# Kernel tuning notes

Measured on AMD Instinct MI355X. Metric: run time of the kernel, lower is better.

Reference implementation:

```python
import jax, jax.numpy as jnp
import numpy as np
import math

NUM_HEADS = 16
HIDDEN = 1024
MLP = 4096
SEQ = 2048
HEAD_DIM = HIDDEN // NUM_HEADS  # 64
EPS = 1e-5


def setup_inputs() -> dict:
    key = jax.random.key(0)
    ks = jax.random.split(key, 16)
    s = 0.02
    inp = {
        "x": jax.random.normal(ks[0], (SEQ, HIDDEN), jnp.float32),
        "rope_cos": jnp.cos(jnp.arange(SEQ, dtype=jnp.float32)[:, None] * (1.0 / (10000.0 ** (jnp.arange(HEAD_DIM // 2, dtype=jnp.float32) * 2 / HEAD_DIM)))[None, :]),
        "rope_sin": jnp.sin(jnp.arange(SEQ, dtype=jnp.float32)[:, None] * (1.0 / (10000.0 ** (jnp.arange(HEAD_DIM // 2, dtype=jnp.float32) * 2 / HEAD_DIM)))[None, :]),
        "norm0_w": jnp.ones((HIDDEN,), jnp.float32),
        "norm0_b": jnp.zeros((HIDDEN,), jnp.float32),
        "norm1_w": jnp.ones((HIDDEN,), jnp.float32),
        "norm1_b": jnp.zeros((HIDDEN,), jnp.float32),
        "wqkv_w": jax.random.normal(ks[1], (3 * HIDDEN, HIDDEN), jnp.float32) * s,
        "wqkv_b": jnp.zeros((3 * HIDDEN,), jnp.float32),
        "wo_w": jax.random.normal(ks[2], (HIDDEN, HIDDEN), jnp.float32) * s,
        "wo_b": jnp.zeros((HIDDEN,), jnp.float32),
        "up_w": jax.random.normal(ks[3], (MLP, HIDDEN), jnp.float32) * s,
        "up_b": jnp.zeros((MLP,), jnp.float32),
        "down_w": jax.random.normal(ks[4], (HIDDEN, MLP), jnp.float32) * s,
        "down_b": jnp.zeros((HIDDEN,), jnp.float32),
        # 4 packed sequences of length 512 each
        "input_row_offsets": jnp.array([0, 512, 1024, 1536, 2048], jnp.int32),
    }
    return inp


def _layernorm(x, w, b):
    m = jnp.mean(x, axis=-1, keepdims=True)
    v = jnp.mean((x - m) ** 2, axis=-1, keepdims=True)
    return (x - m) * jax.lax.rsqrt(v + EPS) * w + b


def _rope(t, cos, sin):
    # t: [S, nh, hd]; cos/sin: [S, hd/2] -> complex rotation of adjacent pairs
    S, nh, hd = t.shape
    t2 = t.reshape(S, nh, hd // 2, 2)
    re, im = t2[..., 0], t2[..., 1]
    c = cos[:, None, :]
    s = sin[:, None, :]
    out = jnp.stack([re * c - im * s, re * s + im * c], axis=-1)
    return out.reshape(S, nh, hd)


def _block(x, rope_cos, rope_sin, norm0_w, norm0_b, wqkv_w, wqkv_b, wo_w, wo_b,
           up_w, up_b, down_w, down_b, norm1_w, norm1_b, input_row_offsets):
    S, H = x.shape
    nh, hd = NUM_HEADS, HEAD_DIM
    h = _layernorm(x, norm0_w, norm0_b)
    qkv = (h @ wqkv_w.T + wqkv_b).reshape(S, 3, nh, hd)
    q, k, v = qkv[:, 0], qkv[:, 1], qkv[:, 2]
    q = _rope(q, rope_cos, rope_sin)
    k = _rope(k, rope_cos, rope_sin)
    # block-diagonal bool mask added as 0/1 float (matches torch `attn_weight += bool_mask`)
    seg = jnp.searchsorted(input_row_offsets, jnp.arange(S), side="right") - 1
    mask = (seg[:, None] == seg[None, :]).astype(jnp.float32)  # [S, S]
    scores = jnp.einsum("shd,thd->hst", q, k) / math.sqrt(hd) + mask[None]
    attn = jax.nn.softmax(scores.astype(jnp.float32), axis=-1).astype(q.dtype)
    out = jnp.einsum("hst,thd->shd", attn, v).reshape(S, H)
    x = x + (out @ wo_w.T + wo_b)
    h = _layernorm(x, norm1_w, norm1_b)
    h = jax.nn.gelu(h @ up_w.T + up_b, approximate=True)
    return x + (h @ down_w.T + down_b)


def reference(x, rope_cos, rope_sin, norm0_w, norm0_b, norm1_w, norm1_b,
              wqkv_w, wqkv_b, wo_w, wo_b, up_w, up_b, down_w, down_b,
              input_row_offsets):
    return _block(x, rope_cos, rope_sin, norm0_w, norm0_b, wqkv_w, wqkv_b,
                  wo_w, wo_b, up_w, up_b, down_w, down_b, norm1_w, norm1_b,
                  input_row_offsets)
```

## Files before the change

### kernel.cpp

```cpp
#include <hip/hip_runtime.h>
#include <hip/hip_bf16.h>
#include <math.h>

#define SEQ 2048
#define HID 1024
#define NH 16
#define HD 64

using f32x4  = __attribute__((ext_vector_type(4))) float;
using bf16x8 = __attribute__((ext_vector_type(8))) short;

union U8 { unsigned int u[4]; bf16x8 v; short s[8]; };

__device__ __forceinline__ short f2bf(float f) {
  unsigned int x = __float_as_uint(f);
  unsigned int r = (x + 0x7fffu + ((x >> 16) & 1u)) >> 16;
  return (short)(r & 0xffffu);
}

__device__ __forceinline__ unsigned int pkbf(float a, float b) {
  return ((unsigned int)(unsigned short)f2bf(a)) |
         (((unsigned int)(unsigned short)f2bf(b)) << 16);
}

__device__ __forceinline__ float bf2f_lo(unsigned int u) {
  return __uint_as_float((u & 0xffffu) << 16);
}
__device__ __forceinline__ float bf2f_hi(unsigned int u) {
  return __uint_as_float(u & 0xffff0000u);
}

__device__ __forceinline__ float fast_exp2(float x) {
#if __has_builtin(__builtin_amdgcn_exp2f)
  return __builtin_amdgcn_exp2f(x);
#else
  return exp2f(x);
#endif
}

__device__ __forceinline__ float fast_rcp(float x) {
#if __has_builtin(__builtin_amdgcn_rcpf)
  return __builtin_amdgcn_rcpf(x);
#else
  return 1.0f / x;
#endif
}

__device__ __forceinline__ void async_cp16(const void* g, void* l) {
  __builtin_amdgcn_global_load_lds(
      (__attribute__((address_space(1))) void*)(g),
      (__attribute__((address_space(3))) void*)(l), 16, 0, 0);
}

__global__ void cvt_all_kernel(const float* __restrict__ a, const float* __restrict__ b,
                               const float* __restrict__ c, const float* __restrict__ d,
                               short* __restrict__ oa, short* __restrict__ ob,
                               short* __restrict__ oc, short* __restrict__ od) {
  int i = blockIdx.x * blockDim.x + threadIdx.x;
  const float* src; short* dst; int off;
  if (i < 786432)        { src = a; dst = oa; off = i; }
  else if (i < 1048576)  { src = b; dst = ob; off = i - 786432; }
  else if (i < 2097152)  { src = c; dst = oc; off = i - 1048576; }
  else                   { src = d; dst = od; off = i - 2097152; }
  float4 v = ((const float4*)src)[off];
  short4 o;
  o.x = f2bf(v.x); o.y = f2bf(v.y); o.z = f2bf(v.z); o.w = f2bf(v.w);
  ((short4*)dst)[off] = o;
}

__global__ __launch_bounds__(256) void ln_kernel(const float* __restrict__ x,
    const float* __restrict__ w, const float* __restrict__ b, short* __restrict__ out) {
  int row = blockIdx.x;
  int tid = threadIdx.x;
  float4 v = ((const float4*)(x + (size_t)row * HID))[tid];
  float s  = v.x + v.y + v.z + v.w;
  float s2 = v.x*v.x + v.y*v.y + v.z*v.z + v.w*v.w;
#pragma unroll
  for (int o = 32; o >= 1; o >>= 1) {
    s  += __shfl_xor(s,  o);
    s2 += __shfl_xor(s2, o);
  }
  __shared__ float red[8];
  int wv = tid >> 6;
  if ((tid & 63) == 0) { red[wv] = s; red[4 + wv] = s2; }
  __syncthreads();
  float ts  = red[0] + red[1] + red[2] + red[3];
  float ts2 = red[4] + red[5] + red[6] + red[7];
  float mean = ts * (1.0f / HID);
  float var  = ts2 * (1.0f / HID) - mean * mean;
  float rs = rsqrtf(var + 1e-5f);
  float4 wv4 = ((const float4*)w)[tid];
  float4 bv4 = ((const float4*)b)[tid];
  short4 o;
  o.x = f2bf((v.x - mean) * rs * wv4.x + bv4.x);
  o.y = f2bf((v.y - mean) * rs * wv4.y + bv4.y);
  o.z = f2bf((v.z - mean) * rs * wv4.z + bv4.z);
  o.w = f2bf((v.w - mean) * rs * wv4.w + bv4.w);
  ((short4*)(out + (size_t)row * HID))[tid] = o;
}

__global__ __launch_bounds__(256) void ropev_kernel(const short* __restrict__ qkvb,
    const float* __restrict__ cosb, const float* __restrict__ sinb,
    short* __restrict__ Qh, short* __restrict__ Kh, short* __restrict__ Vt) {
  __shared__ short tile[64 * 72];
  int s0   = blockIdx.x * 64;
  int head = blockIdx.y;
  int tid  = threadIdx.x;
#pragma unroll
  for (int p = 0; p < 2; p++) {
    int seg = p * 256 + tid;
    int row = seg >> 3;
    int c8  = seg & 7;
    bf16x8 v = *(const bf16x8*)(qkvb + (size_t)(s0 + row) * 3072 + 2048 + head * 64 + c8 * 8);
    *(bf16x8*)(tile + row * 72 + c8 * 8) = v;
  }
  int sl = tid >> 3;
  int c  = tid & 7;
#pragma unroll
  for (int j = 0; j < 2; j++) {
    float scale = (j == 0) ? 0.18033688011112043f : 1.0f;
    short* dstm = (j == 0) ? Qh : Kh;
#pragma unroll
    for (int half = 0; half < 2; half++) {
      int s = s0 + half * 32 + sl;
      uint4 uu = *(const uint4*)(qkvb + (size_t)s * 3072 + j * 1024 + head * 64 + c * 8);
      float4 cs = *(const float4*)(cosb + s * 32 + c * 4);
      float4 sn = *(const float4*)(sinb + s * 32 + c * 4);
      uint4 oo;
      {
        float a = bf2f_lo(uu.x), b = bf2f_hi(uu.x);
        oo.x = pkbf(scale * (a * cs.x - b * sn.x), scale * (a * sn.x + b * cs.x));
        a = bf2f_lo(uu.y); b = bf2f_hi(uu.y);
        oo.y = pkbf(scale * (a * cs.y - b * sn.y), scale * (a * sn.y + b * cs.y));
        a = bf2f_lo(uu.z); b = bf2f_hi(uu.z);
        oo.z = pkbf(scale * (a * cs.z - b * sn.z), scale * (a * sn.z + b * cs.z));
        a = bf2f_lo(uu.w); b = bf2f_hi(uu.w);
        oo.w = pkbf(scale * (a * cs.w - b * sn.w), scale * (a * sn.w + b * cs.w));
      }
      *(uint4*)(dstm + ((size_t)head * SEQ + s) * HD + c * 8) = oo;
    }
  }
  __syncthreads();
#pragma unroll
  for (int p = 0; p < 2; p++) {
    int seg = p * 256 + tid;
    int d   = seg >> 3;
    int sc  = seg & 7;
    U8 o;
#pragma unroll
    for (int jj = 0; jj < 8; jj++) o.s[jj] = tile[(sc * 8 + jj) * 72 + d];
    *(bf16x8*)(Vt + ((size_t)head * HD + d) * SEQ + s0 + sc * 8) = o.v;
  }
}

template <int EPI>
__global__ __launch_bounds__(256) void gemm_bt_kernel(
    const short* __restrict__ A, const short* __restrict__ B,
    const float* __restrict__ bias, const float* __restrict__ resid,
    void* __restrict__ outp, int M, int N, int Klen, int Kstride) {
  __shared__ __attribute__((aligned(16))) short Alds[128 * 64];
  __shared__ __attribute__((aligned(16))) short Blds[128 * 64];
  int tid = threadIdx.x;
  int w    = tid >> 6;
  int lane = tid & 63;
  int lcol  = lane & 15;
  int lhalf = lane >> 4;
  int m0 = blockIdx.y * 128;
  int n0 = blockIdx.x * 128;
  int z  = blockIdx.z;
  int wm = (w & 1) * 64;
  int wn = (w >> 1) * 64;

  const short* apt[4];
  const short* bpt[4];
#pragma unroll
  for (int p = 0; p < 4; p++) {
    int seg = p * 256 + tid;
    int row = seg >> 3;
    int c   = (seg & 7) ^ (row & 7);
    apt[p] = A + (size_t)z * Klen + (size_t)(m0 + row) * Kstride + c * 8;
    bpt[p] = B + (size_t)z * Klen + (size_t)(n0 + row) * Kstride + c * 8;
  }

  f32x4 acc[4][4];
#pragma unroll
  for (int i = 0; i < 4; i++)
#pragma unroll
    for (int j = 0; j < 4; j++) acc[i][j] = (f32x4){0.f, 0.f, 0.f, 0.f};

  for (int k0 = 0; k0 < Klen; k0 += 64) {
#pragma unroll
    for (int p = 0; p < 4; p++) {
      async_cp16(apt[p], Alds + p * 2048 + w * 512);  apt[p] += 64;
      async_cp16(bpt[p], Blds + p * 2048 + w * 512);  bpt[p] += 64;
    }
    __syncthreads();
#pragma unroll
    for (int kc = 0; kc < 2; kc++) {
      bf16x8 af[4], bfr[4];
#pragma unroll
      for (int i = 0; i < 4; i++) {
        int row = wm + i * 16 + lcol;
        af[i] = *(const bf16x8*)(Alds + row * 64 + (((kc * 4 + lhalf) ^ (row & 7)) * 8));
      }
#pragma unroll
      for (int j = 0; j < 4; j++) {
        int row = wn + j * 16 + lcol;
        bfr[j] = *(const bf16x8*)(Blds + row * 64 + (((kc * 4 + lhalf) ^ (row & 7)) * 8));
      }
#pragma unroll
      for (int i = 0; i < 4; i++)
#pragma unroll
        for (int j = 0; j < 4; j++)
          acc[i][j] = __builtin_amdgcn_mfma_f32_16x16x32_bf16(af[i], bfr[j], acc[i][j], 0, 0, 0);
    }
    __syncthreads();
  }

#pragma unroll
  for (int i = 0; i < 4; i++) {
#pragma unroll
    for (int j = 0; j < 4; j++) {
#pragma unroll
      for (int r = 0; r < 4; r++) {
        int row = m0 + wm + i * 16 + lhalf * 4 + r;
        int col = n0 + wn + j * 16 + lcol;
        float v = acc[i][j][r];
        if (EPI != 5) v += bias[col];
        if (EPI == 2) {
          float t = v * (1.5957691216057308f + 0.07135481283942279f * v * v);
          float e = fast_exp2(t * -1.4426950408889634f);
          v = v * fast_rcp(1.0f + e);
          ((short*)outp)[(size_t)row * N + col] = f2bf(v);
        } else if (EPI == 3) {
          ((short*)outp)[(size_t)row * N + col] = f2bf(v);
        } else {
          ((short*)outp)[(size_t)z * M * N + (size_t)row * N + col] = f2bf(v);
        }
      }
    }
  }
}

__global__ __launch_bounds__(256) void attn_kernel(
    const short* __restrict__ Qh, const short* __restrict__ Kh,
    const short* __restrict__ Vt, const int* __restrict__ offs,
    short* __restrict__ Opart, float* __restrict__ Lpart) {
  __shared__ __attribute__((aligned(16))) short Klds[64 * 64];
  __shared__ __attribute__((aligned(16))) short Vlds[64 * 64];
  __shared__ __attribute__((aligned(16))) unsigned int Plds[4][16 * 34];
  int head = blockIdx.y;
  int q0   = blockIdx.x * 64;
  int z    = blockIdx.z;
  int tid  = threadIdx.x;
  int w    = tid >> 6;
  int lane = tid & 63;
  int lcol = lane & 15;
  int h    = lane >> 4;
  int s7   = lcol & 7;
  int o1 = offs[1], o2 = offs[2], o3 = offs[3];

  int qrow = q0 + w * 16 + lcol;
  const short* qb = Qh + ((size_t)head * SEQ + qrow) * HD;
  bf16x8 qf0 = *(const bf16x8*)(qb + h * 8);
  bf16x8 qf1 = *(const bf16x8*)(qb + 32 + h * 8);
  int sq = (qrow >= o1) + (qrow >= o2) + (qrow >= o3);
  U8 qe;
  qe.u[0] = 0; qe.u[1] = 0; qe.u[2] = 0; qe.u[3] = 0;
  if (h == 0) qe.s[sq] = (short)0x3FB9;

  bf16x8 ones;
#pragma unroll
  for (int i = 0; i < 8; i++) ones[i] = 0x3F80;

  int kb0 = lcol * 64 + ((h ^ s7) * 8);
  int kb1 = lcol * 64 + (((4 + h) ^ s7) * 8);
  int vb0 = kb0, vb1 = kb1;
  int pwb = lcol * 34 + h * 2;
  int prb = lcol * 34 + h * 4;

  int tbeg = z * 512;
  const short* kp0; const short* kp1; const short* vp0; const short* vp1;
  {
    int seg = tid, row = seg >> 3, g = (seg & 7) ^ (row & 7);
    kp0 = Kh + ((size_t)head * SEQ + tbeg + row) * HD + g * 8;
    vp0 = Vt + ((size_t)head * HD + row) * SEQ + tbeg + g * 8;
    seg = 256 + tid; row = seg >> 3; g = (seg & 7) ^ (row & 7);
    kp1 = Kh + ((size_t)head * SEQ + tbeg + row) * HD + g * 8;
    vp1 = Vt + ((size_t)head * HD + row) * SEQ + tbeg + g * 8;
  }

  f32x4 o_acc[4];
#pragma unroll
  for (int nt = 0; nt < 4; nt++) o_acc[nt] = (f32x4){0.f, 0.f, 0.f, 0.f};
  f32x4 acc_l = (f32x4){0.f, 0.f, 0.f, 0.f};

  for (int t0 = 0; t0 < 512; t0 += 64) {
    async_cp16(kp0, Klds + w * 512);          kp0 += 64 * HD;
    async_cp16(kp1, Klds + 2048 + w * 512);   kp1 += 64 * HD;
    async_cp16(vp0, Vlds + w * 512);          vp0 += 64;
    async_cp16(vp1, Vlds + 2048 + w * 512);   vp1 += 64;
    __syncthreads();

#pragma unroll
    for (int n = 0; n < 4; n++) {
      bf16x8 kf0 = *(const bf16x8*)(Klds + n * 1024 + kb0);
      bf16x8 kf1 = *(const bf16x8*)(Klds + n * 1024 + kb1);
      int key = tbeg + t0 + n * 16 + lcol;
      int sk = (key >= o1) + (key >= o2) + (key >= o3);
      U8 ke;
      ke.u[0] = (h == 0) ? ((sk == 0) ? 0x00003F80u : (sk == 1) ? 0x3F800000u : 0u) : 0u;
      ke.u[1] = (h == 0) ? ((sk == 2) ? 0x00003F80u : (sk == 3) ? 0x3F800000u : 0u) : 0u;
      ke.u[2] = 0; ke.u[3] = 0;

      f32x4 sacc = (f32x4){0.f, 0.f, 0.f, 0.f};
      sacc = __builtin_amdgcn_mfma_f32_16x16x32_bf16(kf0, qf0, sacc, 0, 0, 0);
      sacc = __builtin_amdgcn_mfma_f32_16x16x32_bf16(kf1, qf1, sacc, 0, 0, 0);
      sacc = __builtin_amdgcn_mfma_f32_16x16x32_bf16(ke.v, qe.v, sacc, 0, 0, 0);

      float p0 = fast_exp2(sacc[0]);
      float p1 = fast_exp2(sacc[1]);
      float p2 = fast_exp2(sacc[2]);
      float p3 = fast_exp2(sacc[3]);
      uint2 pw;
      pw.x = __builtin_amdgcn_perm(__float_as_uint(p1), __float_as_uint(p0), 0x07060302);
      pw.y = __builtin_amdgcn_perm(__float_as_uint(p3), __float_as_uint(p2), 0x07060302);
      *(uint2*)&Plds[w][pwb + n * 8] = pw;
    }

#pragma unroll
    for (int kc = 0; kc < 2; kc++) {
      uint2 a = *(const uint2*)&Plds[w][prb + kc * 16];
      uint2 b = *(const uint2*)&Plds[w][prb + kc * 16 + 2];
      U8 pu;
      pu.u[0] = a.x; pu.u[1] = a.y; pu.u[2] = b.x; pu.u[3] = b.y;
      int vb = kc ? vb1 : vb0;
#pragma unroll
      for (int nt = 0; nt < 4; nt++) {
        bf16x8 vf = *(const bf16x8*)(Vlds + nt * 1024 + vb);
        o_acc[nt] = __builtin_amdgcn_mfma_f32_16x16x32_bf16(vf, pu.v, o_acc[nt], 0, 0, 0);
      }
      acc_l = __builtin_amdgcn_mfma_f32_16x16x32_bf16(ones, pu.v, acc_l, 0, 0, 0);
    }
    __syncthreads();
  }

  short* op = Opart + ((size_t)z * SEQ + qrow) * HID + head * HD + h * 4;
#pragma unroll
  for (int nt = 0; nt < 4; nt++) {
    uint2 ua;
    ua.x = pkbf(o_acc[nt][0], o_acc[nt][1]);
    ua.y = pkbf(o_acc[nt][2], o_acc[nt][3]);
    *(uint2*)(op + nt * 16) = ua;
  }
  if (lane < 16)
    Lpart[((size_t)z * NH + head) * SEQ + qrow] = acc_l[0];
}

__global__ __launch_bounds__(256) void attn_merge_kernel(
    const short* __restrict__ Opart, const float* __restrict__ Lpart,
    short* __restrict__ attn) {
  int i = blockIdx.x * blockDim.x + threadIdx.x;
  int col4 = i & 255;
  int row  = i >> 8;
  int head = col4 >> 4;
  float acc0 = 0.f, acc1 = 0.f, acc2 = 0.f, acc3 = 0.f, l = 0.f;
#pragma unroll
  for (int zz = 0; zz < 4; zz++) {
    uint2 p = ((const uint2*)(Opart + (size_t)zz * SEQ * HID))[i];
    acc0 += bf2f_lo(p.x); acc1 += bf2f_hi(p.x);
    acc2 += bf2f_lo(p.y); acc3 += bf2f_hi(p.y);
    l += Lpart[((size_t)zz * NH + head) * SEQ + row];
  }
  float rl = fast_rcp(l);
  uint2 o;
  o.x = pkbf(acc0 * rl, acc1 * rl);
  o.y = pkbf(acc2 * rl, acc3 * rl);
  ((uint2*)attn)[i] = o;
}

__global__ __launch_bounds__(256) void merge_ln_kernel(
    const short* __restrict__ part, const float* __restrict__ bias,
    const float* __restrict__ resid, const float* __restrict__ w,
    const float* __restrict__ b, float* __restrict__ x1, short* __restrict__ h1) {
  int row = blockIdx.x;
  int tid = threadIdx.x;
  size_t idx = (size_t)row * HID / 4 + tid;
  float4 v = {0.f, 0.f, 0.f, 0.f};
#pragma unroll
  for (int z = 0; z < 4; z++) {
    uint2 p = ((const uint2*)(part + (size_t)z * SEQ * HID))[idx];
    v.x += bf2f_lo(p.x); v.y += bf2f_hi(p.x);
    v.z += bf2f_lo(p.y); v.w += bf2f_hi(p.y);
  }
  float4 bi = ((const float4*)bias)[tid];
  float4 rs4 = ((const float4*)(resid + (size_t)row * HID))[tid];
  v.x += bi.x + rs4.x; v.y += bi.y + rs4.y; v.z += bi.z + rs4.z; v.w += bi.w + rs4.w;
  ((float4*)(x1 + (size_t)row * HID))[tid] = v;
  float s  = v.x + v.y + v.z + v.w;
  float s2 = v.x*v.x + v.y*v.y + v.z*v.z + v.w*v.w;
#pragma unroll
  for (int o = 32; o >= 1; o >>= 1) {
    s  += __shfl_xor(s,  o);
    s2 += __shfl_xor(s2, o);
  }
  __shared__ float red[8];
  int wv = tid >> 6;
  if ((tid & 63) == 0) { red[wv] = s; red[4 + wv] = s2; }
  __syncthreads();
  float ts  = red[0] + red[1] + red[2] + red[3];
  float ts2 = red[4] + red[5] + red[6] + red[7];
  float mean = ts * (1.0f / HID);
  float var  = ts2 * (1.0f / HID) - mean * mean;
  float rsq = rsqrtf(var + 1e-5f);
  float4 wv4 = ((const float4*)w)[tid];
  float4 bv4 = ((const float4*)b)[tid];
  short4 o;
  o.x = f2bf((v.x - mean) * rsq * wv4.x + bv4.x);
  o.y = f2bf((v.y - mean) * rsq * wv4.y + bv4.y);
  o.z = f2bf((v.z - mean) * rsq * wv4.z + bv4.z);
  o.w = f2bf((v.w - mean) * rsq * wv4.w + bv4.w);
  ((short4*)(h1 + (size_t)row * HID))[tid] = o;
}

__global__ __launch_bounds__(256) void merge_bias_kernel(
    const short* __restrict__ part, const float* __restrict__ bias,
    const float* __restrict__ resid, float* __restrict__ out) {
  int i = blockIdx.x * blockDim.x + threadIdx.x;
  int col4 = i & 255;
  float4 v = {0.f, 0.f, 0.f, 0.f};
#pragma unroll
  for (int z = 0; z < 4; z++) {
    uint2 p = ((const uint2*)(part + (size_t)z * SEQ * HID))[i];
    v.x += bf2f_lo(p.x); v.y += bf2f_hi(p.x);
    v.z += bf2f_lo(p.y); v.w += bf2f_hi(p.y);
  }
  float4 bi = ((const float4*)bias)[col4];
  float4 rs = ((const float4*)resid)[i];
  float4 o;
  o.x = v.x + bi.x + rs.x;
  o.y = v.y + bi.y + rs.y;
  o.z = v.z + bi.z + rs.z;
  o.w = v.w + bi.w + rs.w;
  ((float4*)out)[i] = o;
}

extern "C" void kernel_launch(void* const* d_in, const int* in_sizes, int n_in,
                              void* d_out, int out_size, void* d_ws, size_t ws_size,
                              hipStream_t stream) {
  const float* x      = (const float*)d_in[0];
  const float* ropec  = (const float*)d_in[1];
  const float* ropes  = (const float*)d_in[2];
  const float* n0w    = (const float*)d_in[3];
  const float* n0b    = (const float*)d_in[4];
  const float* n1w    = (const float*)d_in[5];
  const float* n1b    = (const float*)d_in[6];
  const float* wqkv_w = (const float*)d_in[7];
  const float* wqkv_b = (const float*)d_in[8];
  const float* wo_w   = (const float*)d_in[9];
  const float* wo_b   = (const float*)d_in[10];
  const float* up_w   = (const float*)d_in[11];
  const float* up_b   = (const float*)d_in[12];
  const float* down_w = (const float*)d_in[13];
  const float* down_b = (const float*)d_in[14];
  const int*   offs   = (const int*)d_in[15];
  float* out = (float*)d_out;

  char* base = (char*)d_ws;
  short* wqkv_bf = (short*)(base + 0);
  short* wo_bf   = (short*)(base + 6291456);
  short* up_bf   = (short*)(base + 8388608);
  short* down_bf = (short*)(base + 16777216);
  short* h0      = (short*)(base + 25165824);
  short* qkv_bf  = (short*)(base + 29360128);
  short* Qh      = (short*)(base + 41943040);
  short* Kh      = (short*)(base + 46137344);
  short* Vt      = (short*)(base + 50331648);
  short* Opart   = (short*)(base + 54525952);
  float* Lpart   = (float*)(base + 71303168);
  short* attn    = (short*)(base + 71827456);
  float* x1      = (float*)(base + 76021760);
  short* h1      = (short*)(base + 84410368);
  short* wopart  = (short*)(base + 25165824);
  short* u       = (short*)(base + 25165824);
  short* dnpart  = (short*)(base + 41943040);

  cvt_all_kernel<<<12288, 256, 0, stream>>>(wqkv_w, wo_w, up_w, down_w,
                                            wqkv_bf, wo_bf, up_bf, down_bf);
  ln_kernel<<<2048, 256, 0, stream>>>(x, n0w, n0b, h0);
  gemm_bt_kernel<3><<<dim3(24, 16), 256, 0, stream>>>(h0, wqkv_bf, wqkv_b, nullptr,
                                                      qkv_bf, 2048, 3072, 1024, 1024);
  ropev_kernel<<<dim3(32, 16), 256, 0, stream>>>(qkv_bf, ropec, ropes, Qh, Kh, Vt);
  attn_kernel<<<dim3(32, 16, 4), 256, 0, stream>>>(Qh, Kh, Vt, offs, Opart, Lpart);
  attn_merge_kernel<<<2048, 256, 0, stream>>>(Opart, Lpart, attn);
  gemm_bt_kernel<5><<<dim3(8, 16, 4), 256, 0, stream>>>(attn, wo_bf, nullptr, nullptr,
                                                        wopart, 2048, 1024, 256, 1024);
  merge_ln_kernel<<<2048, 256, 0, stream>>>(wopart, wo_b, x, n1w, n1b, x1, h1);
  gemm_bt_kernel<2><<<dim3(32, 16), 256, 0, stream>>>(h1, up_bf, up_b, nullptr,
                                                      u, 2048, 4096, 1024, 1024);
  gemm_bt_kernel<5><<<dim3(8, 16, 4), 256, 0, stream>>>(u, down_bf, nullptr, nullptr,
                                                        dnpart, 2048, 1024, 1024, 4096);
  merge_bias_kernel<<<2048, 256, 0, stream>>>(dnpart, down_b, x1, out);
}
```

Before: 272.4 us.

## Double-buffer K/V tiles in attention kernel with async prefetch and MFMA priority

Doubles the K and V shared-memory tiles so the next 64-key block is fetched asynchronously while the current block is computed. Explicit vmcnt waits and raw barriers replace the per-iteration syncthreads. The MFMA sections are also wrapped in s_setprio to favour matrix issue. The goal is to hide global-to-LDS latency inside the attention loop, at the cost of doubled LDS use, which may reduce occupancy.

```diff
diff --git a/kernel.cpp b/kernel.cpp
--- a/kernel.cpp
+++ b/kernel.cpp
@@ -246,8 +246,8 @@
     const short* __restrict__ Qh, const short* __restrict__ Kh,
     const short* __restrict__ Vt, const int* __restrict__ offs,
     short* __restrict__ Opart, float* __restrict__ Lpart) {
-  __shared__ __attribute__((aligned(16))) short Klds[64 * 64];
-  __shared__ __attribute__((aligned(16))) short Vlds[64 * 64];
+  __shared__ __attribute__((aligned(16))) short Klds[2 * 64 * 64];
+  __shared__ __attribute__((aligned(16))) short Vlds[2 * 64 * 64];
   __shared__ __attribute__((aligned(16))) unsigned int Plds[4][16 * 34];
   int head = blockIdx.y;
   int q0   = blockIdx.x * 64;
@@ -295,18 +295,35 @@
   for (int nt = 0; nt < 4; nt++) o_acc[nt] = (f32x4){0.f, 0.f, 0.f, 0.f};
   f32x4 acc_l = (f32x4){0.f, 0.f, 0.f, 0.f};
 
-  for (int t0 = 0; t0 < 512; t0 += 64) {
-    async_cp16(kp0, Klds + w * 512);          kp0 += 64 * HD;
-    async_cp16(kp1, Klds + 2048 + w * 512);   kp1 += 64 * HD;
-    async_cp16(vp0, Vlds + w * 512);          vp0 += 64;
-    async_cp16(vp1, Vlds + 2048 + w * 512);   vp1 += 64;
-    __syncthreads();
+  async_cp16(kp0, Klds + w * 512);          kp0 += 64 * HD;
+  async_cp16(kp1, Klds + 2048 + w * 512);   kp1 += 64 * HD;
+  async_cp16(vp0, Vlds + w * 512);          vp0 += 64;
+  async_cp16(vp1, Vlds + 2048 + w * 512);   vp1 += 64;
+
+  for (int t = 0; t < 8; ++t) {
+    int cur = t & 1;
+    if (t < 7) {
+      int nb = (cur ^ 1) * 4096;
+      async_cp16(kp0, Klds + nb + w * 512);          kp0 += 64 * HD;
+      async_cp16(kp1, Klds + nb + 2048 + w * 512);   kp1 += 64 * HD;
+      async_cp16(vp0, Vlds + nb + w * 512);          vp0 += 64;
+      async_cp16(vp1, Vlds + nb + 2048 + w * 512);   vp1 += 64;
+      asm volatile("s_waitcnt vmcnt(4)" ::: "memory");
+    } else {
+      asm volatile("s_waitcnt vmcnt(0)" ::: "memory");
+    }
+    __builtin_amdgcn_s_barrier();
+    __builtin_amdgcn_sched_barrier(0);
+
+    const short* Kb = Klds + cur * 4096;
+    const short* Vb = Vlds + cur * 4096;
+    int t0 = tbeg + t * 64;
 
 #pragma unroll
     for (int n = 0; n < 4; n++) {
-      bf16x8 kf0 = *(const bf16x8*)(Klds + n * 1024 + kb0);
-      bf16x8 kf1 = *(const bf16x8*)(Klds + n * 1024 + kb1);
-      int key = tbeg + t0 + n * 16 + lcol;
+      bf16x8 kf0 = *(const bf16x8*)(Kb + n * 1024 + kb0);
+      bf16x8 kf1 = *(const bf16x8*)(Kb + n * 1024 + kb1);
+      int key = t0 + n * 16 + lcol;
       int sk = (key >= o1) + (key >= o2) + (key >= o3);
       U8 ke;
       ke.u[0] = (h == 0) ? ((sk == 0) ? 0x00003F80u : (sk == 1) ? 0x3F800000u : 0u) : 0u;
@@ -314,9 +331,11 @@
       ke.u[2] = 0; ke.u[3] = 0;
 
       f32x4 sacc = (f32x4){0.f, 0.f, 0.f, 0.f};
+      __builtin_amdgcn_s_setprio(1);
       sacc = __builtin_amdgcn_mfma_f32_16x16x32_bf16(kf0, qf0, sacc, 0, 0, 0);
       sacc = __builtin_amdgcn_mfma_f32_16x16x32_bf16(kf1, qf1, sacc, 0, 0, 0);
       sacc = __builtin_amdgcn_mfma_f32_16x16x32_bf16(ke.v, qe.v, sacc, 0, 0, 0);
+      __builtin_amdgcn_s_setprio(0);
 
       float p0 = fast_exp2(sacc[0]);
       float p1 = fast_exp2(sacc[1]);
@@ -335,14 +354,17 @@
       U8 pu;
       pu.u[0] = a.x; pu.u[1] = a.y; pu.u[2] = b.x; pu.u[3] = b.y;
       int vb = kc ? vb1 : vb0;
+      __builtin_amdgcn_s_setprio(1);
 #pragma unroll
       for (int nt = 0; nt < 4; nt++) {
-        bf16x8 vf = *(const bf16x8*)(Vlds + nt * 1024 + vb);
+        bf16x8 vf = *(const bf16x8*)(Vb + nt * 1024 + vb);
         o_acc[nt] = __builtin_amdgcn_mfma_f32_16x16x32_bf16(vf, pu.v, o_acc[nt], 0, 0, 0);
       }
       acc_l = __builtin_amdgcn_mfma_f32_16x16x32_bf16(ones, pu.v, acc_l, 0, 0, 0);
-    }
-    __syncthreads();
+      __builtin_amdgcn_s_setprio(0);
+    }
+    __builtin_amdgcn_s_barrier();
+    __builtin_amdgcn_sched_barrier(0);
   }
 
   short* op = Opart + ((size_t)z * SEQ + qrow) * HID + head * HD + h * 4;
```

Result: slower. 297.0 us (+9.0%).

## Double-buffer GEMM LDS tiles to overlap global loads with MFMA

Applied to the files above, without the earlier changes.

Doubles the shared-memory A/B tiles in the bf16 GEMM kernel and prefetches the next K tile asynchronously while the current one is consumed. Explicit vmcnt waits and raw barriers replace __syncthreads, so only the older batch of copies must land before compute. This hides global-memory latency behind MFMA work. In exchange it doubles LDS use to 64 KB per block, which may reduce occupancy, and it relies on manual waitcnt correctness.

```diff
diff --git a/kernel.cpp b/kernel.cpp
--- a/kernel.cpp
+++ b/kernel.cpp
@@ -158,8 +158,8 @@
     const short* __restrict__ A, const short* __restrict__ B,
     const float* __restrict__ bias, const float* __restrict__ resid,
     void* __restrict__ outp, int M, int N, int Klen, int Kstride) {
-  __shared__ __attribute__((aligned(16))) short Alds[128 * 64];
-  __shared__ __attribute__((aligned(16))) short Blds[128 * 64];
+  __shared__ __attribute__((aligned(16))) short Alds[2 * 128 * 64];
+  __shared__ __attribute__((aligned(16))) short Blds[2 * 128 * 64];
   int tid = threadIdx.x;
   int w    = tid >> 6;
   int lane = tid & 63;
@@ -188,25 +188,43 @@
 #pragma unroll
     for (int j = 0; j < 4; j++) acc[i][j] = (f32x4){0.f, 0.f, 0.f, 0.f};
 
-  for (int k0 = 0; k0 < Klen; k0 += 64) {
-#pragma unroll
-    for (int p = 0; p < 4; p++) {
-      async_cp16(apt[p], Alds + p * 2048 + w * 512);  apt[p] += 64;
-      async_cp16(bpt[p], Blds + p * 2048 + w * 512);  bpt[p] += 64;
+  int nk = Klen >> 6;
+
+#pragma unroll
+  for (int p = 0; p < 4; p++) {
+    async_cp16(apt[p], Alds + p * 2048 + w * 512);  apt[p] += 64;
+    async_cp16(bpt[p], Blds + p * 2048 + w * 512);  bpt[p] += 64;
+  }
+
+  for (int kt = 0; kt < nk; ++kt) {
+    int cur = kt & 1;
+    const short* Ab = Alds + cur * 8192;
+    const short* Bb = Blds + cur * 8192;
+    if (kt + 1 < nk) {
+      int nb = (cur ^ 1) * 8192;
+#pragma unroll
+      for (int p = 0; p < 4; p++) {
+        async_cp16(apt[p], Alds + nb + p * 2048 + w * 512);  apt[p] += 64;
+        async_cp16(bpt[p], Blds + nb + p * 2048 + w * 512);  bpt[p] += 64;
+      }
+      asm volatile("s_waitcnt vmcnt(8)" ::: "memory");
+    } else {
+      asm volatile("s_waitcnt vmcnt(0)" ::: "memory");
     }
-    __syncthreads();
+    __builtin_amdgcn_s_barrier();
+    __builtin_amdgcn_sched_barrier(0);
 #pragma unroll
     for (int kc = 0; kc < 2; kc++) {
       bf16x8 af[4], bfr[4];
 #pragma unroll
       for (int i = 0; i < 4; i++) {
         int row = wm + i * 16 + lcol;
-        af[i] = *(const bf16x8*)(Alds + row * 64 + (((kc * 4 + lhalf) ^ (row & 7)) * 8));
+        af[i] = *(const bf16x8*)(Ab + row * 64 + (((kc * 4 + lhalf) ^ (row & 7)) * 8));
       }
 #pragma unroll
       for (int j = 0; j < 4; j++) {
         int row = wn + j * 16 + lcol;
-        bfr[j] = *(const bf16x8*)(Blds + row * 64 + (((kc * 4 + lhalf) ^ (row & 7)) * 8));
+        bfr[j] = *(const bf16x8*)(Bb + row * 64 + (((kc * 4 + lhalf) ^ (row & 7)) * 8));
       }
 #pragma unroll
       for (int i = 0; i < 4; i++)
@@ -214,7 +232,8 @@
         for (int j = 0; j < 4; j++)
           acc[i][j] = __builtin_amdgcn_mfma_f32_16x16x32_bf16(af[i], bfr[j], acc[i][j], 0, 0, 0);
     }
-    __syncthreads();
+    __builtin_amdgcn_s_barrier();
+    __builtin_amdgcn_sched_barrier(0);
   }
 
 #pragma unroll
```

Result: faster. 265.5 us (-2.6%).
